# Kernel tuning notes

Measured on AMD Instinct MI355X. Metric: run time of the kernel, lower is better.

Reference implementation:

```python
import jax, jax.numpy as jnp
import numpy as np

N_GENES = 50000
EMBED = 256
HIDDEN = 256
N_PAIRS = 500000  # undirected interactions -> 2*N_PAIRS directed edges


def setup_inputs() -> dict:
    key = jax.random.key(0)
    ks = jax.random.split(key, 8)
    pairs = jax.random.randint(ks[0], (N_PAIRS, 2), 0, N_GENES)
    a, b = pairs[:, 0], pairs[:, 1]
    # [[a,b],[b,a]] flattened -> symmetric edge_index [2, 2*N_PAIRS]
    edge_index = jnp.stack([jnp.concatenate([a, b]), jnp.concatenate([b, a])]).astype(jnp.int32)
    gene_ind_vec = jax.random.randint(ks[1], (65536,), 0, N_GENES)
    embedding = jax.random.normal(ks[2], (N_GENES, EMBED), dtype=jnp.float32)
    W1 = jax.random.normal(ks[3], (EMBED, HIDDEN), dtype=jnp.float32) * (1.0 / np.sqrt(EMBED))
    b1 = jnp.zeros((HIDDEN,), dtype=jnp.float32)
    W2 = jax.random.normal(ks[4], (HIDDEN, EMBED), dtype=jnp.float32) * (1.0 / np.sqrt(HIDDEN))
    b2 = jnp.zeros((EMBED,), dtype=jnp.float32)
    return {"gene_ind_vec": gene_ind_vec, "edge_index": edge_index,
            "embedding": embedding, "W1": W1, "b1": b1, "W2": W2, "b2": b2}


def gcn_conv(x, src, dst, W, b, n):
    """PyG GCNConv: h = XW; out = D^{-1/2}(A+I)D^{-1/2} h + b."""
    h = x @ W  # [n, out_dim]
    ones_e = jnp.ones(src.shape[0], dtype=x.dtype)
    # degree with self-loops (+1), aggregated at target nodes
    deg = jax.ops.segment_sum(ones_e, dst, num_segments=n) + 1.0
    dinv = jax.lax.rsqrt(deg)
    norm = dinv[src] * dinv[dst]  # [E]
    agg = jax.ops.segment_sum(h[src] * norm[:, None], dst, num_segments=n)
    # self-loop contribution: dinv[i]^2 * h[i]
    return agg + h * (dinv * dinv)[:, None] + b


def reference(gene_ind_vec, edge_index, embedding, W1, b1, W2, b2):
    src, dst = edge_index[0], edge_index[1]
    n = embedding.shape[0]
    # gene_ind_vec only selects device in the original; all-gene embeddings are the node features
    x = gcn_conv(embedding, src, dst, W1, b1, n)
    x = jax.nn.relu(x)  # dropout is identity in eval mode
    x = gcn_conv(x, src, dst, W2, b2, n)
    return x
```

## Files before the change

kernel.cpp:

```cpp
#include <hip/hip_runtime.h>
#include <stdint.h>


typedef unsigned short u16;
typedef __bf16 bf16x8 __attribute__((ext_vector_type(8)));
typedef float f32x4 __attribute__((ext_vector_type(4)));
typedef unsigned short us8 __attribute__((ext_vector_type(8)));
typedef unsigned short us4 __attribute__((ext_vector_type(4)));

#define BSHIFT 8
#define BSTRIDE 6144
#define EPT 8
#define TILE (256 * EPT)

__device__ __forceinline__ float bf2f(u16 u) {
    union { unsigned i; float f; } c;
    c.i = ((unsigned)u) << 16;
    return c.f;
}
__device__ __forceinline__ u16 f2bf(float f) {
    union { float f; unsigned i; } c;
    c.f = f;
    unsigned i = c.i;
    return (u16)((i + 0x7FFF + ((i >> 16) & 1)) >> 16);
}

__global__ __launch_bounds__(256) void scatter_kernel(const int* __restrict__ src,
        const int* __restrict__ dst, int* __restrict__ bcursor,
        int2* __restrict__ rec, int E) {
    __shared__ int cnt[256], lcur[256], gbase[256];
    const int t = threadIdx.x;
    const int base = blockIdx.x * TILE;
    cnt[t] = 0;
    __syncthreads();
    int d[EPT], s[EPT], b[EPT];
#pragma unroll
    for (int k = 0; k < EPT; k++) {
        int e = base + t + k * 256;
        if (e < E) {
            d[k] = dst[e];
            s[k] = src[e];
            b[k] = d[k] >> BSHIFT;
            atomicAdd(&cnt[b[k]], 1);
        } else b[k] = -1;
    }
    __syncthreads();
    int c = cnt[t];
    if (c > 0) gbase[t] = atomicAdd(&bcursor[t], c);
    lcur[t] = 0;
    __syncthreads();
#pragma unroll
    for (int k = 0; k < EPT; k++) {
        if (b[k] >= 0) {
            int r = atomicAdd(&lcur[b[k]], 1);
            rec[(size_t)b[k] * BSTRIDE + gbase[b[k]] + r] = make_int2(d[k], s[k]);
        }
    }
}

__global__ __launch_bounds__(256) void bucket_scan(const int* __restrict__ bcursor,
        int* __restrict__ bbase, int* __restrict__ row_ptr, int NB, int n, int E) {
    __shared__ int sc[256];
    int t = threadIdx.x;
    int v = (t < NB) ? bcursor[t] : 0;
    sc[t] = v;
    __syncthreads();
    for (int off = 1; off < 256; off <<= 1) {
        int u = (t >= off) ? sc[t - off] : 0;
        __syncthreads();
        sc[t] += u;
        __syncthreads();
    }
    if (t < NB) bbase[t] = sc[t] - v;
    if (t == 0) { bbase[NB] = E; row_ptr[n] = E; }
}

__global__ __launch_bounds__(256) void bucket_build(const int2* __restrict__ rec,
        const int* __restrict__ bcursor, const int* __restrict__ bbase,
        int* __restrict__ row_ptr, float* __restrict__ dinv,
        int* __restrict__ csr_src, int n) {
    __shared__ int cnt[256], loff[256], sc[256];
    const int b = blockIdx.x;
    const int t = threadIdx.x;
    const int m = bcursor[b];
    const int base = bbase[b];
    const int2* r = rec + (size_t)b * BSTRIDE;
    cnt[t] = 0;
    __syncthreads();
    for (int i = t; i < m; i += 256)
        atomicAdd(&cnt[r[i].x & 255], 1);
    __syncthreads();
    int c = cnt[t];
    sc[t] = c;
    __syncthreads();
    for (int off = 1; off < 256; off <<= 1) {
        int u = (t >= off) ? sc[t - off] : 0;
        __syncthreads();
        sc[t] += u;
        __syncthreads();
    }
    loff[t] = sc[t] - c;
    int node = (b << BSHIFT) + t;
    if (node < n) {
        row_ptr[node] = base + loff[t];
        dinv[node] = 1.0f / sqrtf((float)c + 1.0f);
    }
    __syncthreads();
    sc[t] = loff[t];
    __syncthreads();
    for (int i = t; i < m; i += 256) {
        int2 e = r[i];
        int idx = atomicAdd(&sc[e.x & 255], 1);
        csr_src[base + idx] = e.y;
    }
}

__global__ void wt_kernel(const float* __restrict__ W, u16* __restrict__ Wt) {
    int t = blockIdx.x * blockDim.x + threadIdx.x;
    int k = t >> 8, nn = t & 255;
    Wt[((size_t)nn << 8) + k] = f2bf(W[t]);
}

template<bool AF32>
__global__ __launch_bounds__(256, 2) void mfma_gemm(const void* __restrict__ Ap,
        const u16* __restrict__ Wt, const float* __restrict__ dinv,
        u16* __restrict__ g, int M) {
    __shared__ u16 Bs[128][264];
    __shared__ u16 As[128][40];
    const int tid = threadIdx.x;
    const int row0 = blockIdx.x * 128;
    const int col0 = blockIdx.y * 128;

    {
        const int col = tid >> 1;
        const int bhalf = tid & 1;
        const u16* srcp = Wt + (((size_t)(col0 + col)) << 8) + bhalf * 128;
#pragma unroll
        for (int q = 0; q < 16; q++)
            *(us8*)&Bs[col][bhalf * 128 + q * 8] = *(const us8*)(srcp + q * 8);
    }

    const int lane = tid & 63;
    const int w = tid >> 6;
    const int wr = w >> 1, wc = w & 1;
    const int l15 = lane & 15, kg = lane >> 4;

    f32x4 acc[4][4];
#pragma unroll
    for (int mi = 0; mi < 4; mi++)
#pragma unroll
        for (int ni = 0; ni < 4; ni++)
            acc[mi][ni] = (f32x4){0.f, 0.f, 0.f, 0.f};

    const int srow = tid >> 1;
    const int shalf = tid & 1;
    const int grow = row0 + srow;

    for (int k0 = 0; k0 < 256; k0 += 32) {
        if (AF32) {
            const float* srcp = (const float*)Ap + ((size_t)grow << 8) + k0 + shalf * 16;
            float4 v[4];
#pragma unroll
            for (int q = 0; q < 4; q++)
                v[q] = (grow < M) ? *(const float4*)(srcp + q * 4)
                                  : make_float4(0.f, 0.f, 0.f, 0.f);
            u16 tmp[16];
#pragma unroll
            for (int q = 0; q < 4; q++) {
                tmp[q * 4 + 0] = f2bf(v[q].x); tmp[q * 4 + 1] = f2bf(v[q].y);
                tmp[q * 4 + 2] = f2bf(v[q].z); tmp[q * 4 + 3] = f2bf(v[q].w);
            }
            *(us8*)&As[srow][shalf * 16]     = *(us8*)&tmp[0];
            *(us8*)&As[srow][shalf * 16 + 8] = *(us8*)&tmp[8];
        } else {
            const u16* srcp = (const u16*)Ap + ((size_t)grow << 8) + k0 + shalf * 16;
            us8 z = {0, 0, 0, 0, 0, 0, 0, 0};
            us8 a0 = (grow < M) ? *(const us8*)srcp       : z;
            us8 a1 = (grow < M) ? *(const us8*)(srcp + 8) : z;
            *(us8*)&As[srow][shalf * 16]     = a0;
            *(us8*)&As[srow][shalf * 16 + 8] = a1;
        }
        __syncthreads();
        bf16x8 af[4], bfv[4];
#pragma unroll
        for (int mi = 0; mi < 4; mi++)
            af[mi] = *(const bf16x8*)&As[wr * 64 + mi * 16 + l15][kg * 8];
#pragma unroll
        for (int ni = 0; ni < 4; ni++)
            bfv[ni] = *(const bf16x8*)&Bs[wc * 64 + ni * 16 + l15][k0 + kg * 8];
#pragma unroll
        for (int mi = 0; mi < 4; mi++)
#pragma unroll
            for (int ni = 0; ni < 4; ni++)
                acc[mi][ni] = __builtin_amdgcn_mfma_f32_16x16x32_bf16(
                    af[mi], bfv[ni], acc[mi][ni], 0, 0, 0);
        __syncthreads();
    }

#pragma unroll
    for (int mi = 0; mi < 4; mi++) {
#pragma unroll
        for (int r = 0; r < 4; r++) {
            int gr = row0 + wr * 64 + mi * 16 + kg * 4 + r;
            if (gr < M) {
                float s = dinv[gr];
                u16* dstp = g + ((size_t)gr << 8) + col0 + wc * 64 + l15;
#pragma unroll
                for (int ni = 0; ni < 4; ni++)
                    dstp[ni * 16] = f2bf(acc[mi][ni][r] * s);
            }
        }
    }
}

template<bool OUT16>
__global__ __launch_bounds__(256) void agg_kernel(const u16* __restrict__ g,
        const int* __restrict__ csr_src, const int* __restrict__ row_ptr,
        const float* __restrict__ dinv, const float* __restrict__ bias,
        void* __restrict__ outp, int n, int do_relu) {
    int wid = threadIdx.x >> 6;
    int lane = threadIdx.x & 63;
    int node = blockIdx.x * 4 + wid;
    if (node >= n) return;
    int jb = row_ptr[node], je = row_ptr[node + 1];
    const size_t co = (size_t)(lane * 4);
    float4 a0 = make_float4(0.f, 0.f, 0.f, 0.f);
    float4 a1 = make_float4(0.f, 0.f, 0.f, 0.f);
    int j = jb;
    for (; j + 8 <= je; j += 8) {
        int s0 = csr_src[j + 0], s1 = csr_src[j + 1];
        int s2 = csr_src[j + 2], s3 = csr_src[j + 3];
        int s4 = csr_src[j + 4], s5 = csr_src[j + 5];
        int s6 = csr_src[j + 6], s7 = csr_src[j + 7];
        ushort4 v0 = *(const ushort4*)(g + ((size_t)s0 << 8) + co);
        ushort4 v1 = *(const ushort4*)(g + ((size_t)s1 << 8) + co);
        ushort4 v2 = *(const ushort4*)(g + ((size_t)s2 << 8) + co);
        ushort4 v3 = *(const ushort4*)(g + ((size_t)s3 << 8) + co);
        ushort4 v4 = *(const ushort4*)(g + ((size_t)s4 << 8) + co);
        ushort4 v5 = *(const ushort4*)(g + ((size_t)s5 << 8) + co);
        ushort4 v6 = *(const ushort4*)(g + ((size_t)s6 << 8) + co);
        ushort4 v7 = *(const ushort4*)(g + ((size_t)s7 << 8) + co);
        a0.x += bf2f(v0.x); a0.y += bf2f(v0.y); a0.z += bf2f(v0.z); a0.w += bf2f(v0.w);
        a1.x += bf2f(v1.x); a1.y += bf2f(v1.y); a1.z += bf2f(v1.z); a1.w += bf2f(v1.w);
        a0.x += bf2f(v2.x); a0.y += bf2f(v2.y); a0.z += bf2f(v2.z); a0.w += bf2f(v2.w);
        a1.x += bf2f(v3.x); a1.y += bf2f(v3.y); a1.z += bf2f(v3.z); a1.w += bf2f(v3.w);
        a0.x += bf2f(v4.x); a0.y += bf2f(v4.y); a0.z += bf2f(v4.z); a0.w += bf2f(v4.w);
        a1.x += bf2f(v5.x); a1.y += bf2f(v5.y); a1.z += bf2f(v5.z); a1.w += bf2f(v5.w);
        a0.x += bf2f(v6.x); a0.y += bf2f(v6.y); a0.z += bf2f(v6.z); a0.w += bf2f(v6.w);
        a1.x += bf2f(v7.x); a1.y += bf2f(v7.y); a1.z += bf2f(v7.z); a1.w += bf2f(v7.w);
    }
    for (; j < je; ++j) {
        int s = csr_src[j];
        ushort4 v = *(const ushort4*)(g + ((size_t)s << 8) + co);
        a0.x += bf2f(v.x); a0.y += bf2f(v.y); a0.z += bf2f(v.z); a0.w += bf2f(v.w);
    }
    ushort4 gd = *(const ushort4*)(g + ((size_t)node << 8) + co);
    float dn = dinv[node];
    float4 bv = *(const float4*)(bias + co);
    float4 o;
    o.x = (a0.x + a1.x + bf2f(gd.x)) * dn + bv.x;
    o.y = (a0.y + a1.y + bf2f(gd.y)) * dn + bv.y;
    o.z = (a0.z + a1.z + bf2f(gd.z)) * dn + bv.z;
    o.w = (a0.w + a1.w + bf2f(gd.w)) * dn + bv.w;
    if (do_relu) {
        o.x = fmaxf(o.x, 0.f); o.y = fmaxf(o.y, 0.f);
        o.z = fmaxf(o.z, 0.f); o.w = fmaxf(o.w, 0.f);
    }
    if (OUT16) {
        us4 ov = { f2bf(o.x), f2bf(o.y), f2bf(o.z), f2bf(o.w) };
        *(us4*)((u16*)outp + ((size_t)node << 8) + co) = ov;
    } else {
        *(float4*)((float*)outp + ((size_t)node << 8) + co) = o;
    }
}

extern "C" void kernel_launch(void* const* d_in, const int* in_sizes, int n_in,
                              void* d_out, int out_size, void* d_ws, size_t ws_size,
                              hipStream_t stream) {
    const int*   edge_index = (const int*)d_in[1];
    const float* embedding  = (const float*)d_in[2];
    const float* W1 = (const float*)d_in[3];
    const float* b1 = (const float*)d_in[4];
    const float* W2 = (const float*)d_in[5];
    const float* b2 = (const float*)d_in[6];
    float* out = (float*)d_out;

    const int E = in_sizes[1] / 2;
    const int n = in_sizes[2] / 256;
    const int* src = edge_index;
    const int* dst = edge_index + E;
    const int NB = (n + 255) >> BSHIFT;

    char* ws = (char*)d_ws;
    int* row_ptr = (int*)ws;    ws += ((size_t)n + 1) * 4;
    float* dinv = (float*)ws;   ws += (size_t)n * 4;
    int* bcursor = (int*)ws;    ws += 256 * 4;
    int* bbase = (int*)ws;      ws += 257 * 4;
    int* csr_src = (int*)ws;    ws += (size_t)E * 4;
    u16* Wt1 = (u16*)ws;        ws += 65536 * 2;
    u16* Wt2 = (u16*)ws;        ws += 65536 * 2;
    ws = (char*)(((uintptr_t)ws + 127) & ~(uintptr_t)127);
    int2* rec = (int2*)ws;      ws += (size_t)NB * BSTRIDE * 8;
    ws = (char*)(((uintptr_t)ws + 127) & ~(uintptr_t)127);
    u16* g = (u16*)ws;
    u16* x1 = (u16*)d_out;

    hipMemsetAsync(bcursor, 0, 256 * 4, stream);
    scatter_kernel<<<(E + TILE - 1) / TILE, 256, 0, stream>>>(src, dst, bcursor, rec, E);
    bucket_scan<<<1, 256, 0, stream>>>(bcursor, bbase, row_ptr, NB, n, E);
    bucket_build<<<NB, 256, 0, stream>>>(rec, bcursor, bbase, row_ptr, dinv, csr_src, n);
    wt_kernel<<<256, 256, 0, stream>>>(W1, Wt1);
    wt_kernel<<<256, 256, 0, stream>>>(W2, Wt2);

    dim3 gg((n + 127) / 128, 2);
    mfma_gemm<true><<<gg, 256, 0, stream>>>(embedding, Wt1, dinv, g, n);
    agg_kernel<true><<<(n + 3) / 4, 256, 0, stream>>>(g, csr_src, row_ptr, dinv, b1, x1, n, 1);
    mfma_gemm<false><<<gg, 256, 0, stream>>>(x1, Wt2, dinv, g, n);
    agg_kernel<false><<<(n + 3) / 4, 256, 0, stream>>>(g, csr_src, row_ptr, dinv, b2, out, n, 0);
}
```

Before: 263.7 us.

## Split aggregation across column groups and edge lanes with shuffle reduction

The aggregation kernel now splits each node's 256 feature columns into 8 column groups, each handled by its own block, for an 8x larger grid. Within a wavefront, four lane groups each take every fourth edge and read 2 bf16 columns per lane, then combine their partial sums with cross-lane shuffles. The aim is more parallelism and memory-level concurrency for low-degree nodes. In exchange, each 64-byte row read becomes many tiny 4-byte accesses, and row_ptr and csr_src are fetched 8 times per node.

```diff
diff --git a/kernel.cpp b/kernel.cpp
--- a/kernel.cpp
+++ b/kernel.cpp
@@ -218,59 +218,52 @@
         const int* __restrict__ csr_src, const int* __restrict__ row_ptr,
         const float* __restrict__ dinv, const float* __restrict__ bias,
         void* __restrict__ outp, int n, int do_relu) {
-    int wid = threadIdx.x >> 6;
-    int lane = threadIdx.x & 63;
-    int node = blockIdx.x * 4 + wid;
+    const int cg = blockIdx.x & 7;
+    const int nb = blockIdx.x >> 3;
+    const int wid = threadIdx.x >> 6;
+    const int lane = threadIdx.x & 63;
+    const int node = nb * 4 + wid;
     if (node >= n) return;
-    int jb = row_ptr[node], je = row_ptr[node + 1];
-    const size_t co = (size_t)(lane * 4);
-    float4 a0 = make_float4(0.f, 0.f, 0.f, 0.f);
-    float4 a1 = make_float4(0.f, 0.f, 0.f, 0.f);
-    int j = jb;
-    for (; j + 8 <= je; j += 8) {
-        int s0 = csr_src[j + 0], s1 = csr_src[j + 1];
-        int s2 = csr_src[j + 2], s3 = csr_src[j + 3];
-        int s4 = csr_src[j + 4], s5 = csr_src[j + 5];
-        int s6 = csr_src[j + 6], s7 = csr_src[j + 7];
-        ushort4 v0 = *(const ushort4*)(g + ((size_t)s0 << 8) + co);
-        ushort4 v1 = *(const ushort4*)(g + ((size_t)s1 << 8) + co);
-        ushort4 v2 = *(const ushort4*)(g + ((size_t)s2 << 8) + co);
-        ushort4 v3 = *(const ushort4*)(g + ((size_t)s3 << 8) + co);
-        ushort4 v4 = *(const ushort4*)(g + ((size_t)s4 << 8) + co);
-        ushort4 v5 = *(const ushort4*)(g + ((size_t)s5 << 8) + co);
-        ushort4 v6 = *(const ushort4*)(g + ((size_t)s6 << 8) + co);
-        ushort4 v7 = *(const ushort4*)(g + ((size_t)s7 << 8) + co);
-        a0.x += bf2f(v0.x); a0.y += bf2f(v0.y); a0.z += bf2f(v0.z); a0.w += bf2f(v0.w);
-        a1.x += bf2f(v1.x); a1.y += bf2f(v1.y); a1.z += bf2f(v1.z); a1.w += bf2f(v1.w);
-        a0.x += bf2f(v2.x); a0.y += bf2f(v2.y); a0.z += bf2f(v2.z); a0.w += bf2f(v2.w);
-        a1.x += bf2f(v3.x); a1.y += bf2f(v3.y); a1.z += bf2f(v3.z); a1.w += bf2f(v3.w);
-        a0.x += bf2f(v4.x); a0.y += bf2f(v4.y); a0.z += bf2f(v4.z); a0.w += bf2f(v4.w);
-        a1.x += bf2f(v5.x); a1.y += bf2f(v5.y); a1.z += bf2f(v5.z); a1.w += bf2f(v5.w);
-        a0.x += bf2f(v6.x); a0.y += bf2f(v6.y); a0.z += bf2f(v6.z); a0.w += bf2f(v6.w);
-        a1.x += bf2f(v7.x); a1.y += bf2f(v7.y); a1.z += bf2f(v7.z); a1.w += bf2f(v7.w);
-    }
-    for (; j < je; ++j) {
-        int s = csr_src[j];
-        ushort4 v = *(const ushort4*)(g + ((size_t)s << 8) + co);
-        a0.x += bf2f(v.x); a0.y += bf2f(v.y); a0.z += bf2f(v.z); a0.w += bf2f(v.w);
-    }
-    ushort4 gd = *(const ushort4*)(g + ((size_t)node << 8) + co);
-    float dn = dinv[node];
-    float4 bv = *(const float4*)(bias + co);
-    float4 o;
-    o.x = (a0.x + a1.x + bf2f(gd.x)) * dn + bv.x;
-    o.y = (a0.y + a1.y + bf2f(gd.y)) * dn + bv.y;
-    o.z = (a0.z + a1.z + bf2f(gd.z)) * dn + bv.z;
-    o.w = (a0.w + a1.w + bf2f(gd.w)) * dn + bv.w;
-    if (do_relu) {
-        o.x = fmaxf(o.x, 0.f); o.y = fmaxf(o.y, 0.f);
-        o.z = fmaxf(o.z, 0.f); o.w = fmaxf(o.w, 0.f);
-    }
-    if (OUT16) {
-        us4 ov = { f2bf(o.x), f2bf(o.y), f2bf(o.z), f2bf(o.w) };
-        *(us4*)((u16*)outp + ((size_t)node << 8) + co) = ov;
-    } else {
-        *(float4*)((float*)outp + ((size_t)node << 8) + co) = o;
+    const int es = lane >> 4;
+    const int cl = lane & 15;
+    const int coff = cg * 32 + cl * 2;
+
+    const int jb = row_ptr[node], je = row_ptr[node + 1];
+    float ax = 0.f, ay = 0.f, bx2 = 0.f, by2 = 0.f;
+    int j = jb + es;
+    for (; j + 4 < je; j += 8) {
+        int s0 = csr_src[j];
+        int s1 = csr_src[j + 4];
+        ushort2 v0 = *(const ushort2*)(g + ((size_t)s0 << 8) + coff);
+        ushort2 v1 = *(const ushort2*)(g + ((size_t)s1 << 8) + coff);
+        ax += bf2f(v0.x); ay += bf2f(v0.y);
+        bx2 += bf2f(v1.x); by2 += bf2f(v1.y);
+    }
+    if (j < je) {
+        int s0 = csr_src[j];
+        ushort2 v0 = *(const ushort2*)(g + ((size_t)s0 << 8) + coff);
+        ax += bf2f(v0.x); ay += bf2f(v0.y);
+    }
+    ax += bx2; ay += by2;
+    if (es == 0) {
+        ushort2 v = *(const ushort2*)(g + ((size_t)node << 8) + coff);
+        ax += bf2f(v.x); ay += bf2f(v.y);
+    }
+    ax += __shfl_xor(ax, 16, 64); ay += __shfl_xor(ay, 16, 64);
+    ax += __shfl_xor(ax, 32, 64); ay += __shfl_xor(ay, 32, 64);
+
+    if (es == 0) {
+        float dn = dinv[node];
+        float ox = ax * dn + bias[coff];
+        float oy = ay * dn + bias[coff + 1];
+        if (do_relu) { ox = fmaxf(ox, 0.f); oy = fmaxf(oy, 0.f); }
+        if (OUT16) {
+            ushort2 ov = { f2bf(ox), f2bf(oy) };
+            *(ushort2*)((u16*)outp + ((size_t)node << 8) + coff) = ov;
+        } else {
+            float2 ov = { ox, oy };
+            *(float2*)((float*)outp + ((size_t)node << 8) + coff) = ov;
+        }
     }
 }
 
@@ -283,7 +276,6 @@
     const float* b1 = (const float*)d_in[4];
     const float* W2 = (const float*)d_in[5];
     const float* b2 = (const float*)d_in[6];
-    float* out = (float*)d_out;
 
     const int E = in_sizes[1] / 2;
     const int n = in_sizes[2] / 256;
@@ -313,8 +305,9 @@
     wt_kernel<<<256, 256, 0, stream>>>(W2, Wt2);
 
     dim3 gg((n + 127) / 128, 2);
+    const int agg_grid = ((n + 3) / 4) * 8;
     mfma_gemm<true><<<gg, 256, 0, stream>>>(embedding, Wt1, dinv, g, n);
-    agg_kernel<true><<<(n + 3) / 4, 256, 0, stream>>>(g, csr_src, row_ptr, dinv, b1, x1, n, 1);
+    agg_kernel<true><<<agg_grid, 256, 0, stream>>>(g, csr_src, row_ptr, dinv, b1, x1, n, 1);
     mfma_gemm<false><<<gg, 256, 0, stream>>>(x1, Wt2, dinv, g, n);
-    agg_kernel<false><<<(n + 3) / 4, 256, 0, stream>>>(g, csr_src, row_ptr, dinv, b2, out, n, 0);
-}
+    agg_kernel<false><<<agg_grid, 256, 0, stream>>>(g, csr_src, row_ptr, dinv, b2, (float*)d_out, n, 0);
+}
```

Measured after the change: 499.6 us. 1.89x slower.
